# Kernel optimization log

Hardware: AMD Instinct MI355X
Metric: run time of the kernel (lower is better)

The kernel has to match this reference:

```python
import jax, jax.numpy as jnp
import numpy as np

N = 50000
E = 800000
IN = 128
C = 32   # out_channels per head
H = 4    # heads
HC = H * C
EDGE_DIM = 1
NEG_SLOPE = 0.2
BN_EPS = 1e-5


def setup_inputs() -> dict:
    key = jax.random.key(0)
    ks = jax.random.split(key, 12)
    glorot = lambda k, shp: (jax.random.uniform(k, shp, jnp.float32, -1.0, 1.0)
                             * jnp.sqrt(6.0 / (shp[0] + shp[-1])))
    return {
        "x": jax.random.normal(ks[0], (N, IN), jnp.float32),
        "edge_index": jax.random.randint(ks[1], (2, E), 0, N, jnp.int64),
        "edge_attr": jax.random.normal(ks[2], (E, EDGE_DIM), jnp.float32),
        # GATv2Conv params
        "W_l": glorot(ks[3], (IN, HC)),   # lin_l (source)
        "b_l": jnp.zeros((HC,), jnp.float32),
        "W_r": glorot(ks[4], (IN, HC)),   # lin_r (target)
        "b_r": jnp.zeros((HC,), jnp.float32),
        "W_e": glorot(ks[5], (EDGE_DIM, HC)),  # lin_edge (no bias)
        "att": glorot(ks[6], (H, C)),
        "bias": jnp.zeros((HC,), jnp.float32),  # final conv bias (concat)
        # BatchNorm1d affine params
        "gamma": jnp.ones((HC,), jnp.float32),
        "beta": jnp.zeros((HC,), jnp.float32),
    }


def reference(x, edge_index, edge_attr, W_l, b_l, W_r, b_r, W_e, att, bias, gamma, beta):
    src = edge_index[0]  # message source j
    dst = edge_index[1]  # message target i (aggregation segment)

    x_l = (x @ W_l + b_l).reshape(N, H, C)  # source transform
    x_r = (x @ W_r + b_r).reshape(N, H, C)  # target transform
    e = (edge_attr @ W_e).reshape(E, H, C)  # edge transform

    # GATv2 attention: LeakyReLU(x_i + x_j + e) . att, per edge & head
    m = jax.nn.leaky_relu(x_l[src] + x_r[dst] + e, NEG_SLOPE)  # [E,H,C]
    alpha = jnp.einsum('ehc,hc->eh', m, att)                   # [E,H]

    # segment softmax over destination nodes (numerically stable)
    amax = jax.ops.segment_max(alpha, dst, num_segments=N)     # [N,H]
    ex = jnp.exp(alpha - amax[dst])
    denom = jax.ops.segment_sum(ex, dst, num_segments=N)       # [N,H]
    alpha = ex / (denom[dst] + 1e-16)

    # scatter-add aggregation of weighted source features
    out = jax.ops.segment_sum(x_l[src] * alpha[:, :, None], dst, num_segments=N)
    out = out.reshape(N, HC) + bias

    # BatchNorm1d (training-mode batch statistics), then ELU; dropout = eval (identity)
    mean = out.mean(axis=0)
    var = out.var(axis=0)
    out = (out - mean) * jax.lax.rsqrt(var + BN_EPS) * gamma + beta
    return jax.nn.elu(out)
```

## Files before the change

kernel.cpp:

```cpp
#include <hip/hip_runtime.h>
#include <math.h>

constexpr int NN  = 50000;
constexpr int NE  = 800000;
constexpr int IND = 128;
constexpr int HCD = 128;

constexpr int NBKT = 250;
constexpr int NPB  = 200;
constexpr int BCAP = 4096;
constexpr int BE   = 1024;
constexpr int EPT  = BE / 256;
constexpr int B1B  = (NE + BE - 1) / BE;

typedef __attribute__((ext_vector_type(8))) short bf16x8;
typedef __attribute__((ext_vector_type(4))) float f32x4;
typedef __attribute__((ext_vector_type(2))) float f32x2;

__device__ __forceinline__ void splitbf(float f, unsigned short &h, unsigned short &lo) {
    unsigned u = __float_as_uint(f);
    h = (unsigned short)(u >> 16);
    float fh = __uint_as_float(u & 0xffff0000u);
    lo = (unsigned short)(__float_as_uint(f - fh) >> 16);
}
__device__ __forceinline__ unsigned short bf16rne(float f) {
    unsigned u = __float_as_uint(f);
    u += 0x7fffu + ((u >> 16) & 1u);
    return (unsigned short)(u >> 16);
}

constexpr int BM = 128;
constexpr int BK = 64;

__global__ __launch_bounds__(256) void gemm_mfma(
    const float* __restrict__ x, const float* __restrict__ Wl,
    const float* __restrict__ Wr, const float* __restrict__ bl,
    const float* __restrict__ br, unsigned short* __restrict__ xlbf,
    unsigned short* __restrict__ xrbf)
{
    extern __shared__ char smem[];
    char* Ah = smem;
    char* Al = smem + 16384;
    char* Bh = smem + 32768;

    const int tid = threadIdx.x;
    const float* W  = blockIdx.y ? Wr : Wl;
    const float* bv = blockIdx.y ? br : bl;
    unsigned short* outp = blockIdx.y ? xrbf : xlbf;
    const int bn = blockIdx.x * BM;

    const int l   = tid & 63;
    const int wid = tid >> 6;
    const int wr  = (wid >> 1) * 64;
    const int wc  = (wid & 1) * 64;
    const int lr  = l & 15;
    const int kg  = l >> 4;

    f32x4 acc[4][4];
#pragma unroll
    for (int s = 0; s < 4; ++s)
#pragma unroll
        for (int f = 0; f < 4; ++f) acc[s][f] = (f32x4){0.f, 0.f, 0.f, 0.f};

    const int cB  = tid & 127;
    const int khB = tid >> 7;

    for (int ki = 0; ki < 2; ++ki) {
#pragma unroll
        for (int r = 0; r < 8; ++r) {
            int g = tid + r * 256;
            int row = g >> 4, k4 = g & 15;
            int node = bn + row;
            float4 v = make_float4(0.f, 0.f, 0.f, 0.f);
            if (node < NN) v = *(const float4*)&x[node * IND + ki * BK + k4 * 4];
            unsigned short h0, h1, h2, h3, q0, q1, q2, q3;
            splitbf(v.x, h0, q0); splitbf(v.y, h1, q1);
            splitbf(v.z, h2, q2); splitbf(v.w, h3, q3);
            int off = (row * BK + k4 * 4) * 2;
            int swz = off ^ ((row & 7) << 4);
            *(ushort4*)(Ah + swz) = make_ushort4(h0, h1, h2, h3);
            *(ushort4*)(Al + swz) = make_ushort4(q0, q1, q2, q3);
        }
#pragma unroll
        for (int r = 0; r < 8; ++r) {
            int kb = r * 8 + khB * 4;
            float f0 = W[(ki * BK + kb + 0) * HCD + cB];
            float f1 = W[(ki * BK + kb + 1) * HCD + cB];
            float f2 = W[(ki * BK + kb + 2) * HCD + cB];
            float f3 = W[(ki * BK + kb + 3) * HCD + cB];
            int off = (cB * BK + kb) * 2;
            int swz = off ^ ((cB & 7) << 4);
            *(ushort4*)(Bh + swz) = make_ushort4(bf16rne(f0), bf16rne(f1),
                                                 bf16rne(f2), bf16rne(f3));
        }
        __syncthreads();
#pragma unroll
        for (int kk = 0; kk < 2; ++kk) {
            bf16x8 Bfh[4];
#pragma unroll
            for (int f = 0; f < 4; ++f) {
                int c = wc + f * 16 + lr;
                int swz = (c * 128 + kk * 64 + kg * 16) ^ ((c & 7) << 4);
                Bfh[f] = *(const bf16x8*)(Bh + swz);
            }
#pragma unroll
            for (int s = 0; s < 4; ++s) {
                int row = wr + s * 16 + lr;
                int swz = (row * 128 + kk * 64 + kg * 16) ^ ((row & 7) << 4);
                bf16x8 Afh = *(const bf16x8*)(Ah + swz);
                bf16x8 Afl = *(const bf16x8*)(Al + swz);
#pragma unroll
                for (int f = 0; f < 4; ++f) {
                    acc[s][f] = __builtin_amdgcn_mfma_f32_16x16x32_bf16(Afh, Bfh[f], acc[s][f], 0, 0, 0);
                    acc[s][f] = __builtin_amdgcn_mfma_f32_16x16x32_bf16(Afl, Bfh[f], acc[s][f], 0, 0, 0);
                }
            }
        }
        __syncthreads();
    }
#pragma unroll
    for (int s = 0; s < 4; ++s)
#pragma unroll
        for (int f = 0; f < 4; ++f) {
            int c = wc + f * 16 + lr;
            float bb = bv[c];
#pragma unroll
            for (int j = 0; j < 4; ++j) {
                int r = bn + wr + s * 16 + kg * 4 + j;
                if (r >= NN) continue;
                outp[r * HCD + c] = bf16rne(acc[s][f][j] + bb);
            }
        }
}

__global__ __launch_bounds__(256) void bucket_kernel(
    const int* __restrict__ src, const int* __restrict__ dst,
    const float* __restrict__ ea, int* __restrict__ gcur,
    int2* __restrict__ stg)
{
    __shared__ int cnt[NBKT], base[NBKT];
    const int tid = threadIdx.x;
    for (int j = tid; j < NBKT; j += 256) cnt[j] = 0;
    __syncthreads();

    const int e0 = blockIdx.x * BE;
    int w0[EPT], w1[EPT]; int nb[EPT];
#pragma unroll
    for (int j = 0; j < EPT; ++j) {
        int e = e0 + j * 256 + tid;
        bool ok = e < NE;
        int s_ = ok ? src[e] : 0;
        int d_ = ok ? dst[e] : 0;
        float a_ = ok ? ea[e] : 0.f;
        int b  = d_ / NPB;
        int dl = d_ - b * NPB;
        w0[j] = s_ | (dl << 17);
        w1[j] = __float_as_int(a_);
        nb[j] = ok ? b : -1;
        if (ok) atomicAdd(&cnt[b], 1);
    }
    __syncthreads();
    for (int j = tid; j < NBKT; j += 256) {
        base[j] = cnt[j] ? atomicAdd(&gcur[j], cnt[j]) : 0;
        cnt[j] = 0;
    }
    __syncthreads();
#pragma unroll
    for (int j = 0; j < EPT; ++j) {
        if (nb[j] >= 0) {
            int slot = base[nb[j]] + atomicAdd(&cnt[nb[j]], 1);
            if (slot < BCAP)
                stg[nb[j] * BCAP + slot] = make_int2(w0[j], w1[j]);
        }
    }
}

__global__ __launch_bounds__(256) void bscan(const int* __restrict__ gcur,
                                             int* __restrict__ bbase,
                                             int* __restrict__ off)
{
    __shared__ int t[256];
    int tid = threadIdx.x;
    int v = (tid < NBKT) ? gcur[tid] : 0;
    t[tid] = v;
    __syncthreads();
    for (int d = 1; d < 256; d <<= 1) {
        int u = (tid >= d) ? t[tid - d] : 0;
        __syncthreads();
        t[tid] += u;
        __syncthreads();
    }
    if (tid < NBKT) bbase[tid] = t[tid] - v;
    if (tid == 0) off[NN] = NE;
}

__global__ __launch_bounds__(256) void csr_build(
    const int2* __restrict__ stg, const int* __restrict__ gcur,
    const int* __restrict__ bbase, int* __restrict__ off,
    int2* __restrict__ csr)
{
    __shared__ int hist[NPB], t[256], cur[NPB];
    const int b = blockIdx.x, tid = threadIdx.x;
    const int count = min(gcur[b], BCAP);
    const int base  = bbase[b];

    if (tid < NPB) { hist[tid] = 0; cur[tid] = 0; }
    __syncthreads();
    for (int sl = tid; sl < count; sl += 256)
        atomicAdd(&hist[(unsigned)stg[b * BCAP + sl].x >> 17], 1);
    __syncthreads();

    int hv = (tid < NPB) ? hist[tid] : 0;
    t[tid] = hv;
    __syncthreads();
    for (int d = 1; d < 256; d <<= 1) {
        int u = (tid >= d) ? t[tid - d] : 0;
        __syncthreads();
        t[tid] += u;
        __syncthreads();
    }
    if (tid < NPB) off[b * NPB + tid] = base + t[tid] - hv;
    __syncthreads();

    for (int sl = tid; sl < count; sl += 256) {
        int2 v = stg[b * BCAP + sl];
        int dl = (unsigned)v.x >> 17;
        int pos = base + (t[dl] - hist[dl]) + atomicAdd(&cur[dl], 1);
        csr[pos] = make_int2(v.x & 0x1ffff, v.y);
    }
}

__global__ __launch_bounds__(256) void node_kernel(
    const unsigned short* __restrict__ xlbf, const unsigned short* __restrict__ xrbf,
    const float* __restrict__ We, const float* __restrict__ att,
    const int* __restrict__ off, const int2* __restrict__ csr,
    unsigned short* __restrict__ out_bf)
{
    const int n = blockIdx.x * 4 + (threadIdx.x >> 6);
    if (n >= NN) return;
    const int l  = threadIdx.x & 63;
    const int g  = l >> 4;
    const int i  = l & 15;
    const int c0 = i * 8;

    f32x2 wev[4], atv[4];
#pragma unroll
    for (int j = 0; j < 4; ++j) {
        wev[j] = (f32x2){We[c0 + 2 * j], We[c0 + 2 * j + 1]};
        atv[j] = (f32x2){att[c0 + 2 * j], att[c0 + 2 * j + 1]};
    }

    uint4 xru = *(const uint4*)&xrbf[n * HCD + c0];
    f32x2 xrv[4];
    xrv[0] = (f32x2){__uint_as_float(xru.x << 16), __uint_as_float(xru.x & 0xffff0000u)};
    xrv[1] = (f32x2){__uint_as_float(xru.y << 16), __uint_as_float(xru.y & 0xffff0000u)};
    xrv[2] = (f32x2){__uint_as_float(xru.z << 16), __uint_as_float(xru.z & 0xffff0000u)};
    xrv[3] = (f32x2){__uint_as_float(xru.w << 16), __uint_as_float(xru.w & 0xffff0000u)};

    const int s = off[n], e = off[n + 1];
    if (s == e) {
        if (g == 0)
            *(uint4*)&out_bf[n * HCD + c0] = make_uint4(0, 0, 0, 0);
        return;
    }

    float mx = -3.0e38f, sm = 0.f;
    f32x2 acc[4];
#pragma unroll
    for (int j = 0; j < 4; ++j) acc[j] = (f32x2){0.f, 0.f};

    int k = s;
    int2 c2; uint4 xb; bool v;
    {
        int idx = min(k + g, e - 1);
        c2 = csr[idx];
        xb = *(const uint4*)&xlbf[c2.x * HCD + c0];
        v  = (k + g) < e;
    }

    for (; k < e; k += 4) {
        int2 c2n; uint4 xbn; bool vn;
        {
            int idx = min(k + 4 + g, e - 1);
            c2n = csr[idx];
            xbn = *(const uint4*)&xlbf[c2n.x * HCD + c0];
            vn  = (k + 4 + g) < e;
        }
        f32x2 xv[4];
        xv[0] = (f32x2){__uint_as_float(xb.x << 16), __uint_as_float(xb.x & 0xffff0000u)};
        xv[1] = (f32x2){__uint_as_float(xb.y << 16), __uint_as_float(xb.y & 0xffff0000u)};
        xv[2] = (f32x2){__uint_as_float(xb.z << 16), __uint_as_float(xb.z & 0xffff0000u)};
        xv[3] = (f32x2){__uint_as_float(xb.w << 16), __uint_as_float(xb.w & 0xffff0000u)};

        float eaf = __int_as_float(c2.y);
        f32x2 p2 = (f32x2){0.f, 0.f};
#pragma unroll
        for (int j = 0; j < 4; ++j) {
            f32x2 s2 = xv[j] + xrv[j];
            s2 = eaf * wev[j] + s2;
            f32x2 m2 = __builtin_elementwise_max(s2, s2 * 0.2f);
            p2 = m2 * atv[j] + p2;
        }
        float p = p2.x + p2.y;
        p += __shfl_xor(p, 1);
        p += __shfl_xor(p, 2);
        if (!v) p = -1.0e30f;

        if (__any(p > mx + 8.f)) {
            float nm = fmaxf(mx, p);
            float sc = __expf(mx - nm);
            sm *= sc;
#pragma unroll
            for (int j = 0; j < 4; ++j) acc[j] *= sc;
            mx = nm;
        }
        float ev = v ? __expf(p - mx) : 0.f;
        sm += ev;
#pragma unroll
        for (int j = 0; j < 4; ++j) acc[j] = ev * xv[j] + acc[j];

        c2 = c2n; xb = xbn; v = vn;
    }

    float M = fmaxf(mx, __shfl_xor(mx, 16));
    M = fmaxf(M, __shfl_xor(M, 32));
    float sc = __expf(mx - M);
    float smT = sm * sc;
    smT += __shfl_xor(smT, 16);
    smT += __shfl_xor(smT, 32);
    float inv = 1.f / (smT + 1e-16f);
    unsigned uo[4];
#pragma unroll
    for (int j = 0; j < 4; ++j) {
        float a0 = acc[j].x * sc, a1 = acc[j].y * sc;
        a0 += __shfl_xor(a0, 16);  a0 += __shfl_xor(a0, 32);
        a1 += __shfl_xor(a1, 16);  a1 += __shfl_xor(a1, 32);
        uo[j] = (unsigned)bf16rne(a0 * inv) | ((unsigned)bf16rne(a1 * inv) << 16);
    }
    if (g == 0)
        *(uint4*)&out_bf[n * HCD + c0] = make_uint4(uo[0], uo[1], uo[2], uo[3]);
}

__global__ __launch_bounds__(256) void bnstat_kernel(const unsigned short* __restrict__ out_bf,
                                                     float* __restrict__ stats)
{
    __shared__ float lsum[HCD], lsq[HCD];
    const int tid = threadIdx.x;
    if (tid < HCD) { lsum[tid] = 0.f; lsq[tid] = 0.f; }
    __syncthreads();

    const int q  = tid & 31;
    const int c0 = q * 4;
    const int r  = tid >> 5;

    float s[4] = {0.f, 0.f, 0.f, 0.f}, qq[4] = {0.f, 0.f, 0.f, 0.f};
    for (int n = blockIdx.x * 8 + r; n < NN; n += gridDim.x * 8) {
        uint2 u = *(const uint2*)&out_bf[(size_t)n * HCD + c0];
        float v0 = __uint_as_float(u.x << 16);
        float v1 = __uint_as_float(u.x & 0xffff0000u);
        float v2 = __uint_as_float(u.y << 16);
        float v3 = __uint_as_float(u.y & 0xffff0000u);
        s[0] += v0; qq[0] += v0 * v0;
        s[1] += v1; qq[1] += v1 * v1;
        s[2] += v2; qq[2] += v2 * v2;
        s[3] += v3; qq[3] += v3 * v3;
    }
#pragma unroll
    for (int j = 0; j < 4; ++j) {
        s[j]  += __shfl_xor(s[j], 32);
        qq[j] += __shfl_xor(qq[j], 32);
    }
    if ((tid & 32) == 0) {
#pragma unroll
        for (int j = 0; j < 4; ++j) {
            atomicAdd(&lsum[c0 + j], s[j]);
            atomicAdd(&lsq[c0 + j], qq[j]);
        }
    }
    __syncthreads();
    if (tid < HCD)            atomicAdd(&stats[tid], lsum[tid]);
    else                      atomicAdd(&stats[tid], lsq[tid - HCD]);
}

__global__ __launch_bounds__(128) void bnprep_kernel(
    const float* __restrict__ stats, const float* __restrict__ gamma,
    const float* __restrict__ beta, float* __restrict__ ss)
{
    int c = threadIdx.x;
    float mean = stats[c] * (1.f / NN);
    float var  = stats[HCD + c] * (1.f / NN) - mean * mean;
    float sc   = gamma[c] * rsqrtf(var + 1e-5f);
    ss[c]       = sc;
    ss[HCD + c] = beta[c] - mean * sc;
}

__global__ __launch_bounds__(256) void bn_elu_kernel(
    const unsigned short* __restrict__ out_bf, const float* __restrict__ ss,
    float* __restrict__ out)
{
    int i8 = blockIdx.x * 256 + threadIdx.x;
    if (i8 >= NN * HCD / 8) return;
    int c0 = (i8 & 15) * 8;
    uint4 u = *(const uint4*)&out_bf[(size_t)i8 * 8];
    float vv[8] = {
        __uint_as_float(u.x << 16), __uint_as_float(u.x & 0xffff0000u),
        __uint_as_float(u.y << 16), __uint_as_float(u.y & 0xffff0000u),
        __uint_as_float(u.z << 16), __uint_as_float(u.z & 0xffff0000u),
        __uint_as_float(u.w << 16), __uint_as_float(u.w & 0xffff0000u)};
    float o[8];
#pragma unroll
    for (int j = 0; j < 8; ++j) {
        int c = c0 + j;
        float t = fmaf(vv[j], ss[c], ss[HCD + c]);
        o[j] = (t > 0.f) ? t : (__expf(t) - 1.f);
    }
    float* dst = &out[(size_t)i8 * 8];
    *(float4*)dst       = make_float4(o[0], o[1], o[2], o[3]);
    *(float4*)(dst + 4) = make_float4(o[4], o[5], o[6], o[7]);
}

extern "C" void kernel_launch(void* const* d_in, const int* in_sizes, int n_in,
                              void* d_out, int out_size, void* d_ws, size_t ws_size,
                              hipStream_t stream)
{
    (void)in_sizes; (void)n_in; (void)out_size; (void)ws_size;
    const float* x    = (const float*)d_in[0];
    const int*   ei   = (const int*)  d_in[1];
    const float* ea   = (const float*)d_in[2];
    const float* Wl   = (const float*)d_in[3];
    const float* bl   = (const float*)d_in[4];
    const float* Wr   = (const float*)d_in[5];
    const float* br   = (const float*)d_in[6];
    const float* We   = (const float*)d_in[7];
    const float* att  = (const float*)d_in[8];
    const float* gamma= (const float*)d_in[10];
    const float* beta = (const float*)d_in[11];
    float* out = (float*)d_out;

    char* wsb = (char*)d_ws;
    size_t o = 0;
    auto take = [&](size_t bytes) -> char* {
        char* p = wsb + o;
        o += (bytes + 255) & ~size_t(255);
        return p;
    };
    unsigned short* xlbf  = (unsigned short*)take(sizeof(unsigned short) * NN * HCD);
    unsigned short* xrbf  = (unsigned short*)take(sizeof(unsigned short) * NN * HCD);
    unsigned short* outbf = (unsigned short*)take(sizeof(unsigned short) * NN * HCD);
    int2*  csr     = (int2*) take(sizeof(int2)  * NE);
    int*   offs    = (int*)  take(sizeof(int)   * (NN + 1));
    int*   bbase   = (int*)  take(sizeof(int)   * 256);
    int2*  stg     = (int2*) take(sizeof(int2)  * NBKT * BCAP);
    float* ss      = (float*)take(sizeof(float) * 2 * HCD);
    size_t zbytes  = sizeof(float) * 2 * HCD + sizeof(int) * NBKT;
    char*  zbase   = take(zbytes);
    float* stats   = (float*)zbase;
    int*   gcur    = (int*)(stats + 2 * HCD);

    hipMemsetAsync(zbase, 0, zbytes, stream);

    const int* srcI = ei;
    const int* dstI = ei + NE;

    gemm_mfma<<<dim3((NN + BM - 1) / BM, 2), 256, 49152, stream>>>(
        x, Wl, Wr, bl, br, xlbf, xrbf);
    bucket_kernel<<<B1B, 256, 0, stream>>>(srcI, dstI, ea, gcur, stg);
    bscan<<<1, 256, 0, stream>>>(gcur, bbase, offs);
    csr_build<<<NBKT, 256, 0, stream>>>(stg, gcur, bbase, offs, csr);
    node_kernel<<<(NN + 3) / 4, 256, 0, stream>>>(xlbf, xrbf, We, att, offs, csr, outbf);
    bnstat_kernel<<<512, 256, 0, stream>>>(outbf, stats);
    bnprep_kernel<<<1, 128, 0, stream>>>(stats, gamma, beta, ss);
    bn_elu_kernel<<<(NN * HCD / 8 + 255) / 256, 256, 0, stream>>>(outbf, ss, out);
}
```

Before: 146.8 us.

## Fuse both projections per GEMM block, pack CSR entries, deepen gather prefetch

The GEMM now computes both x@W_l and x@W_r in one block: each wave pair selects one weight tile, so the x tile is loaded and split into bf16 hi/lo only once, at the cost of 64KB of LDS and twice the accumulators. CSR entries shrink from an 8-byte int2 to a 4-byte word holding a 16-bit source index plus the edge attribute rounded to bf16. This halves CSR traffic in the node kernel but lowers edge-attribute precision and relies on node ids fitting in 16 bits. The node kernel's software prefetch goes from one to two edge-groups ahead to hide gather latency, which uses more registers.

```diff
diff --git a/kernel.cpp b/kernel.cpp
--- a/kernel.cpp
+++ b/kernel.cpp
@@ -39,28 +39,26 @@
     unsigned short* __restrict__ xrbf)
 {
     extern __shared__ char smem[];
-    char* Ah = smem;
-    char* Al = smem + 16384;
-    char* Bh = smem + 32768;
+    char* Ah  = smem;
+    char* Al  = smem + 16384;
+    char* Bh0 = smem + 32768;
+    char* Bh1 = smem + 49152;
 
     const int tid = threadIdx.x;
-    const float* W  = blockIdx.y ? Wr : Wl;
-    const float* bv = blockIdx.y ? br : bl;
-    unsigned short* outp = blockIdx.y ? xrbf : xlbf;
     const int bn = blockIdx.x * BM;
 
-    const int l   = tid & 63;
-    const int wid = tid >> 6;
-    const int wr  = (wid >> 1) * 64;
-    const int wc  = (wid & 1) * 64;
-    const int lr  = l & 15;
-    const int kg  = l >> 4;
-
-    f32x4 acc[4][4];
+    const int l    = tid & 63;
+    const int wid  = tid >> 6;
+    const int wrow = (wid >> 1) * 64;
+    const int wsel = wid & 1;
+    const int lr   = l & 15;
+    const int kg   = l >> 4;
+
+    f32x4 acc[4][8];
 #pragma unroll
     for (int s = 0; s < 4; ++s)
 #pragma unroll
-        for (int f = 0; f < 4; ++f) acc[s][f] = (f32x4){0.f, 0.f, 0.f, 0.f};
+        for (int f = 0; f < 8; ++f) acc[s][f] = (f32x4){0.f, 0.f, 0.f, 0.f};
 
     const int cB  = tid & 127;
     const int khB = tid >> 7;
@@ -84,49 +82,56 @@
 #pragma unroll
         for (int r = 0; r < 8; ++r) {
             int kb = r * 8 + khB * 4;
-            float f0 = W[(ki * BK + kb + 0) * HCD + cB];
-            float f1 = W[(ki * BK + kb + 1) * HCD + cB];
-            float f2 = W[(ki * BK + kb + 2) * HCD + cB];
-            float f3 = W[(ki * BK + kb + 3) * HCD + cB];
             int off = (cB * BK + kb) * 2;
             int swz = off ^ ((cB & 7) << 4);
-            *(ushort4*)(Bh + swz) = make_ushort4(bf16rne(f0), bf16rne(f1),
-                                                 bf16rne(f2), bf16rne(f3));
-        }
-        __syncthreads();
+            *(ushort4*)(Bh0 + swz) = make_ushort4(
+                bf16rne(Wl[(ki * BK + kb + 0) * HCD + cB]),
+                bf16rne(Wl[(ki * BK + kb + 1) * HCD + cB]),
+                bf16rne(Wl[(ki * BK + kb + 2) * HCD + cB]),
+                bf16rne(Wl[(ki * BK + kb + 3) * HCD + cB]));
+            *(ushort4*)(Bh1 + swz) = make_ushort4(
+                bf16rne(Wr[(ki * BK + kb + 0) * HCD + cB]),
+                bf16rne(Wr[(ki * BK + kb + 1) * HCD + cB]),
+                bf16rne(Wr[(ki * BK + kb + 2) * HCD + cB]),
+                bf16rne(Wr[(ki * BK + kb + 3) * HCD + cB]));
+        }
+        __syncthreads();
+        const char* Bh = wsel ? Bh1 : Bh0;
 #pragma unroll
         for (int kk = 0; kk < 2; ++kk) {
-            bf16x8 Bfh[4];
-#pragma unroll
-            for (int f = 0; f < 4; ++f) {
-                int c = wc + f * 16 + lr;
+            bf16x8 Bf[8];
+#pragma unroll
+            for (int f = 0; f < 8; ++f) {
+                int c = f * 16 + lr;
                 int swz = (c * 128 + kk * 64 + kg * 16) ^ ((c & 7) << 4);
-                Bfh[f] = *(const bf16x8*)(Bh + swz);
+                Bf[f] = *(const bf16x8*)(Bh + swz);
             }
 #pragma unroll
             for (int s = 0; s < 4; ++s) {
-                int row = wr + s * 16 + lr;
+                int row = wrow + s * 16 + lr;
                 int swz = (row * 128 + kk * 64 + kg * 16) ^ ((row & 7) << 4);
                 bf16x8 Afh = *(const bf16x8*)(Ah + swz);
                 bf16x8 Afl = *(const bf16x8*)(Al + swz);
 #pragma unroll
-                for (int f = 0; f < 4; ++f) {
-                    acc[s][f] = __builtin_amdgcn_mfma_f32_16x16x32_bf16(Afh, Bfh[f], acc[s][f], 0, 0, 0);
-                    acc[s][f] = __builtin_amdgcn_mfma_f32_16x16x32_bf16(Afl, Bfh[f], acc[s][f], 0, 0, 0);
+                for (int f = 0; f < 8; ++f) {
+                    acc[s][f] = __builtin_amdgcn_mfma_f32_16x16x32_bf16(Afh, Bf[f], acc[s][f], 0, 0, 0);
+                    acc[s][f] = __builtin_amdgcn_mfma_f32_16x16x32_bf16(Afl, Bf[f], acc[s][f], 0, 0, 0);
                 }
             }
         }
         __syncthreads();
     }
+    unsigned short* outp = wsel ? xrbf : xlbf;
+    const float* bv = wsel ? br : bl;
 #pragma unroll
     for (int s = 0; s < 4; ++s)
 #pragma unroll
-        for (int f = 0; f < 4; ++f) {
-            int c = wc + f * 16 + lr;
+        for (int f = 0; f < 8; ++f) {
+            int c = f * 16 + lr;
             float bb = bv[c];
 #pragma unroll
             for (int j = 0; j < 4; ++j) {
-                int r = bn + wr + s * 16 + kg * 4 + j;
+                int r = bn + wrow + s * 16 + kg * 4 + j;
                 if (r >= NN) continue;
                 outp[r * HCD + c] = bf16rne(acc[s][f][j] + bb);
             }
@@ -154,7 +159,7 @@
         float a_ = ok ? ea[e] : 0.f;
         int b  = d_ / NPB;
         int dl = d_ - b * NPB;
-        w0[j] = s_ | (dl << 17);
+        w0[j] = s_ | (dl << 16);
         w1[j] = __float_as_int(a_);
         nb[j] = ok ? b : -1;
         if (ok) atomicAdd(&cnt[b], 1);
@@ -197,7 +202,7 @@
 __global__ __launch_bounds__(256) void csr_build(
     const int2* __restrict__ stg, const int* __restrict__ gcur,
     const int* __restrict__ bbase, int* __restrict__ off,
-    int2* __restrict__ csr)
+    unsigned* __restrict__ csr)
 {
     __shared__ int hist[NPB], t[256], cur[NPB];
     const int b = blockIdx.x, tid = threadIdx.x;
@@ -207,7 +212,7 @@
     if (tid < NPB) { hist[tid] = 0; cur[tid] = 0; }
     __syncthreads();
     for (int sl = tid; sl < count; sl += 256)
-        atomicAdd(&hist[(unsigned)stg[b * BCAP + sl].x >> 17], 1);
+        atomicAdd(&hist[(unsigned)stg[b * BCAP + sl].x >> 16], 1);
     __syncthreads();
 
     int hv = (tid < NPB) ? hist[tid] : 0;
@@ -224,16 +229,17 @@
 
     for (int sl = tid; sl < count; sl += 256) {
         int2 v = stg[b * BCAP + sl];
-        int dl = (unsigned)v.x >> 17;
+        int dl = (unsigned)v.x >> 16;
         int pos = base + (t[dl] - hist[dl]) + atomicAdd(&cur[dl], 1);
-        csr[pos] = make_int2(v.x & 0x1ffff, v.y);
+        csr[pos] = (unsigned)(v.x & 0xffff)
+                 | ((unsigned)bf16rne(__int_as_float(v.y)) << 16);
     }
 }
 
 __global__ __launch_bounds__(256) void node_kernel(
     const unsigned short* __restrict__ xlbf, const unsigned short* __restrict__ xrbf,
     const float* __restrict__ We, const float* __restrict__ att,
-    const int* __restrict__ off, const int2* __restrict__ csr,
+    const int* __restrict__ off, const unsigned* __restrict__ csr,
     unsigned short* __restrict__ out_bf)
 {
     const int n = blockIdx.x * 4 + (threadIdx.x >> 6);
@@ -270,29 +276,33 @@
     for (int j = 0; j < 4; ++j) acc[j] = (f32x2){0.f, 0.f};
 
     int k = s;
-    int2 c2; uint4 xb; bool v;
+    unsigned cA, cB; uint4 xA, xB; bool vA, vB;
     {
         int idx = min(k + g, e - 1);
-        c2 = csr[idx];
-        xb = *(const uint4*)&xlbf[c2.x * HCD + c0];
-        v  = (k + g) < e;
+        cA = csr[idx];
+        xA = *(const uint4*)&xlbf[(cA & 0xffffu) * HCD + c0];
+        vA = (k + g) < e;
+        idx = min(k + 4 + g, e - 1);
+        cB = csr[idx];
+        xB = *(const uint4*)&xlbf[(cB & 0xffffu) * HCD + c0];
+        vB = (k + 4 + g) < e;
     }
 
     for (; k < e; k += 4) {
-        int2 c2n; uint4 xbn; bool vn;
+        unsigned cC; uint4 xC; bool vC;
         {
-            int idx = min(k + 4 + g, e - 1);
-            c2n = csr[idx];
-            xbn = *(const uint4*)&xlbf[c2n.x * HCD + c0];
-            vn  = (k + 4 + g) < e;
+            int idx = min(k + 8 + g, e - 1);
+            cC = csr[idx];
+            xC = *(const uint4*)&xlbf[(cC & 0xffffu) * HCD + c0];
+            vC = (k + 8 + g) < e;
         }
         f32x2 xv[4];
-        xv[0] = (f32x2){__uint_as_float(xb.x << 16), __uint_as_float(xb.x & 0xffff0000u)};
-        xv[1] = (f32x2){__uint_as_float(xb.y << 16), __uint_as_float(xb.y & 0xffff0000u)};
-        xv[2] = (f32x2){__uint_as_float(xb.z << 16), __uint_as_float(xb.z & 0xffff0000u)};
-        xv[3] = (f32x2){__uint_as_float(xb.w << 16), __uint_as_float(xb.w & 0xffff0000u)};
-
-        float eaf = __int_as_float(c2.y);
+        xv[0] = (f32x2){__uint_as_float(xA.x << 16), __uint_as_float(xA.x & 0xffff0000u)};
+        xv[1] = (f32x2){__uint_as_float(xA.y << 16), __uint_as_float(xA.y & 0xffff0000u)};
+        xv[2] = (f32x2){__uint_as_float(xA.z << 16), __uint_as_float(xA.z & 0xffff0000u)};
+        xv[3] = (f32x2){__uint_as_float(xA.w << 16), __uint_as_float(xA.w & 0xffff0000u)};
+
+        float eaf = __uint_as_float(cA & 0xffff0000u);
         f32x2 p2 = (f32x2){0.f, 0.f};
 #pragma unroll
         for (int j = 0; j < 4; ++j) {
@@ -304,7 +314,7 @@
         float p = p2.x + p2.y;
         p += __shfl_xor(p, 1);
         p += __shfl_xor(p, 2);
-        if (!v) p = -1.0e30f;
+        if (!vA) p = -1.0e30f;
 
         if (__any(p > mx + 8.f)) {
             float nm = fmaxf(mx, p);
@@ -314,12 +324,13 @@
             for (int j = 0; j < 4; ++j) acc[j] *= sc;
             mx = nm;
         }
-        float ev = v ? __expf(p - mx) : 0.f;
+        float ev = vA ? __expf(p - mx) : 0.f;
         sm += ev;
 #pragma unroll
         for (int j = 0; j < 4; ++j) acc[j] = ev * xv[j] + acc[j];
 
-        c2 = c2n; xb = xbn; v = vn;
+        cA = cB; xA = xB; vA = vB;
+        cB = cC; xB = xC; vB = vC;
     }
 
     float M = fmaxf(mx, __shfl_xor(mx, 16));
@@ -447,7 +458,7 @@
     unsigned short* xlbf  = (unsigned short*)take(sizeof(unsigned short) * NN * HCD);
     unsigned short* xrbf  = (unsigned short*)take(sizeof(unsigned short) * NN * HCD);
     unsigned short* outbf = (unsigned short*)take(sizeof(unsigned short) * NN * HCD);
-    int2*  csr     = (int2*) take(sizeof(int2)  * NE);
+    unsigned* csr  = (unsigned*)take(sizeof(unsigned) * NE);
     int*   offs    = (int*)  take(sizeof(int)   * (NN + 1));
     int*   bbase   = (int*)  take(sizeof(int)   * 256);
     int2*  stg     = (int2*) take(sizeof(int2)  * NBKT * BCAP);
@@ -462,7 +473,7 @@
     const int* srcI = ei;
     const int* dstI = ei + NE;
 
-    gemm_mfma<<<dim3((NN + BM - 1) / BM, 2), 256, 49152, stream>>>(
+    gemm_mfma<<<(NN + BM - 1) / BM, 256, 65536, stream>>>(
         x, Wl, Wr, bl, br, xlbf, xrbf);
     bucket_kernel<<<B1B, 256, 0, stream>>>(srcI, dstI, ea, gcur, stg);
     bscan<<<1, 256, 0, stream>>>(gcur, bbase, offs);
```

Result: slower. 163.3 us (+11.3%).
